# Performance work log

Hardware: AMD Instinct MI355X
Metric: run time of the kernel (lower is better)

Reference implementation:

```python
import jax, jax.numpy as jnp
import numpy as np

E = 32          # num_experts
K = 4           # num_experts_per_tok
H = 1024        # hidden_size
I = 768         # moe_intermediate_size
ROUTED_SCALING_FACTOR = 1.0


def setup_inputs() -> dict:
    key = jax.random.key(0)
    k0, k1, k2, k3, k4, k5 = jax.random.split(key, 6)
    return {
        "hidden_states": jax.random.normal(k0, (1, 2048, H), jnp.float32),
        "gate_w": jax.random.normal(k1, (E, H), jnp.float32) * 0.02,
        "w1": jax.random.normal(k2, (E, H, I), jnp.float32) * 0.02,   # gate proj per expert
        "w3": jax.random.normal(k3, (E, H, I), jnp.float32) * 0.02,   # up proj per expert
        "w2": jax.random.normal(k4, (E, I, H), jnp.float32) * 0.02,   # down proj per expert
        "e_bias": jax.random.normal(k5, (E,), jnp.float32) * 0.02,    # e_score_correction_bias
    }


def reference(hidden_states, gate_w, w1, w3, w2, e_bias):
    orig_shape = hidden_states.shape
    x = hidden_states.reshape(-1, orig_shape[-1])            # [T, H]
    T = x.shape[0]

    # ----- router gate (ReplicatedLinear, no bias) -----
    router_logits = x @ gate_w.T                             # [T, E]

    # ----- grouped top-k with num_expert_group=1, topk_group=1 == plain top-k
    # scoring_func='sigmoid'; correction bias only affects expert *selection*,
    # the routing weights are the uncorrected sigmoid scores.
    scores = jax.nn.sigmoid(router_logits.astype(jnp.float32))          # [T, E]
    _, topk_ids = jax.lax.top_k(scores + e_bias[None, :], K)            # [T, K]
    topk_w = jnp.take_along_axis(scores, topk_ids, axis=1)              # [T, K]
    # renormalize (norm_topk_prob=True)
    topk_w = topk_w / jnp.sum(topk_w, axis=1, keepdims=True)

    # dense combine weights [T, E] (zero for unselected experts)
    combine = jnp.zeros((T, E), jnp.float32).at[jnp.arange(T)[:, None], topk_ids].add(topk_w)

    # ----- experts: SwiGLU per expert, combine weighted -----
    g = jnp.einsum("th,ehi->tei", x, w1)                     # [T, E, I]
    u = jnp.einsum("th,ehi->tei", x, w3)                     # [T, E, I]
    a = jax.nn.silu(g) * u * combine[:, :, None].astype(x.dtype)
    out = jnp.einsum("tei,eih->th", a, w2)                   # [T, H]

    out = out * ROUTED_SCALING_FACTOR
    return out.reshape(orig_shape)
```

## Files before the change

### kernel.cpp

```cpp
#include <hip/hip_runtime.h>
#include <cstdint>

#define TOK 2048
#define HD  1024
#define ID  768
#define NE  32

typedef unsigned short u16t;
typedef unsigned int   u32t;
typedef __bf16 bf16x8 __attribute__((ext_vector_type(8)));
typedef float  f32x4  __attribute__((ext_vector_type(4)));
typedef u16t   u16x8  __attribute__((ext_vector_type(8)));
typedef u16t   u16x4  __attribute__((ext_vector_type(4)));
typedef float  fvec4  __attribute__((ext_vector_type(4)));

__device__ __forceinline__ u16t f2b(float f) {
  u32t u = __float_as_uint(f);
  u32t r = u + 0x7fffu + ((u >> 16) & 1u);
  return (u16t)(r >> 16);
}

__device__ __forceinline__ int swz(int row, int kc) {
  return (row * 4 + (kc ^ ((row >> 2) & 3))) * 8;
}

__global__ void k_cvt(const float* __restrict__ x, u16t* __restrict__ xb) {
  int i = (blockIdx.x * 256 + threadIdx.x) * 4;
  fvec4 v = *(const fvec4*)(x + i);
  u16x4 o = { f2b(v[0]), f2b(v[1]), f2b(v[2]), f2b(v[3]) };
  *(u16x4*)(xb + i) = o;
}

__global__ void k_router(const float* __restrict__ x, const float* __restrict__ gw,
                         const float* __restrict__ eb,
                         int* __restrict__ topk_ids, float* __restrict__ topk_w,
                         int* __restrict__ counts) {
  int lane = threadIdx.x & 63;
  int t = blockIdx.x * 4 + (threadIdx.x >> 6);
  const float* xt = x + (size_t)t * HD;
  float myscore = 0.f;
  for (int e = 0; e < NE; ++e) {
    const float* ge = gw + (size_t)e * HD;
    float s = 0.f;
#pragma unroll
    for (int i = 0; i < HD / 64; ++i) s = fmaf(xt[lane + i * 64], ge[lane + i * 64], s);
#pragma unroll
    for (int off = 32; off; off >>= 1) s += __shfl_xor(s, off);
    if (lane == e) myscore = s;
  }
  float sig = 1.f / (1.f + expf(-myscore));
  float biased = (lane < NE) ? (sig + eb[lane]) : -3.0e38f;
  float wsum = 0.f;
  int ids[4]; float wsv[4];
#pragma unroll
  for (int k = 0; k < 4; ++k) {
    float v = biased; int idx = lane;
#pragma unroll
    for (int off = 32; off; off >>= 1) {
      float ov = __shfl_xor(v, off);
      int   oi = __shfl_xor(idx, off);
      if (ov > v || (ov == v && oi < idx)) { v = ov; idx = oi; }
    }
    ids[k] = idx;
    float sc = __shfl(sig, idx);
    wsv[k] = sc; wsum += sc;
    if (lane == idx) biased = -3.0e38f;
  }
  float inv = 1.f / wsum;
#pragma unroll
  for (int k = 0; k < 4; ++k) {
    if (lane == k) {
      topk_ids[t * 4 + k] = ids[k];
      topk_w[t * 4 + k]  = wsv[k] * inv;
      atomicAdd(&counts[ids[k]], 1);
    }
  }
}

__global__ void k_bucket(const int* __restrict__ topk_ids, const float* __restrict__ topk_w,
                         const int* __restrict__ counts, int* __restrict__ offsets,
                         int* __restrict__ pairTok, float* __restrict__ pairW,
                         int* __restrict__ invp) {
  __shared__ int soff[NE + 1];
  __shared__ int scur[NE];
  int tid = threadIdx.x;
  if (tid == 0) {
    int acc = 0;
    for (int e = 0; e < NE; ++e) { soff[e] = acc; acc += counts[e]; }
    soff[NE] = acc;
  }
  if (tid < NE) scur[tid] = 0;
  __syncthreads();
  if (tid <= NE) offsets[tid] = soff[tid];
  for (int p = tid; p < TOK * 4; p += 256) {
    int e = topk_ids[p];
    int pos = soff[e] + atomicAdd(&scur[e], 1);
    pairTok[pos] = p;
    pairW[pos]   = topk_w[p];
    invp[p]      = pos;
  }
}

__launch_bounds__(256, 2)
__global__ void k_gemm1(const u16t* __restrict__ xb, const float* __restrict__ w1,
                        const float* __restrict__ w3,
                        const int* __restrict__ counts, const int* __restrict__ offsets,
                        const int* __restrict__ pairTok, const float* __restrict__ pairW,
                        u16t* __restrict__ A) {
  const int e = blockIdx.y;
  const int colbase = blockIdx.x * 64;
  const int count = counts[e];
  const int base  = offsets[e];
  const int tid = threadIdx.x, lane = tid & 63, wv = tid >> 6;

  __shared__ __align__(16) u16t Xs[256 * 32];
  __shared__ __align__(16) u16t Ws2[2][64 * 32];
  __shared__ float pw[256];
  __shared__ int   prow[256];

  const float* w1e = w1 + (size_t)e * HD * ID;
  const float* w3e = w3 + (size_t)e * HD * ID;

  for (int r0 = 0; r0 < count; r0 += 256) {
    __syncthreads();
    {
      int idx = r0 + tid;
      bool valid = idx < count;
      prow[tid] = valid ? (pairTok[base + idx] >> 2) : -1;
      pw[tid]   = valid ? pairW[base + idx] : 0.f;
    }
    f32x4 zz = {0.f, 0.f, 0.f, 0.f};
    f32x4 accg[4][4], accu[4][4];
#pragma unroll
    for (int a = 0; a < 4; ++a)
#pragma unroll
      for (int b = 0; b < 4; ++b) { accg[a][b] = zz; accu[a][b] = zz; }

    for (int kk = 0; kk < HD; kk += 32) {
      {
        int tok = prow[tid];
        u16x8 d0 = {0,0,0,0,0,0,0,0}, d1 = d0, d2 = d0, d3 = d0;
        if (tok >= 0) {
          const u16t* src = xb + (size_t)tok * HD + kk;
          d0 = *(const u16x8*)(src);
          d1 = *(const u16x8*)(src + 8);
          d2 = *(const u16x8*)(src + 16);
          d3 = *(const u16x8*)(src + 24);
        }
        *(u16x8*)&Xs[swz(tid, 0)] = d0;
        *(u16x8*)&Xs[swz(tid, 1)] = d1;
        *(u16x8*)&Xs[swz(tid, 2)] = d2;
        *(u16x8*)&Xs[swz(tid, 3)] = d3;
      }
      {
        const float* wp = (tid < 128) ? w1e : w3e;
        u16t* wsp = &Ws2[tid >> 7][0];
        int u = tid & 127;
        int cg = u & 15, hg = u >> 4;
        const float* src = wp + (size_t)(kk + hg * 4) * ID + colbase + cg * 4;
        fvec4 v0 = *(const fvec4*)(src);
        fvec4 v1 = *(const fvec4*)(src + ID);
        fvec4 v2 = *(const fvec4*)(src + 2 * ID);
        fvec4 v3 = *(const fvec4*)(src + 3 * ID);
        int kc = hg >> 1, half = (hg & 1) * 4;
#pragma unroll
        for (int c = 0; c < 4; ++c) {
          int col = cg * 4 + c;
          u16x4 pk = { f2b(v0[c]), f2b(v1[c]), f2b(v2[c]), f2b(v3[c]) };
          *(u16x4*)&wsp[swz(col, kc) + half] = pk;
        }
      }
      __syncthreads();
      bf16x8 af[4], b1f[4], b3f[4];
      int kcl = lane >> 4;
      int rb = wv * 64 + (lane & 15);
#pragma unroll
      for (int rf = 0; rf < 4; ++rf)
        af[rf] = *(const bf16x8*)&Xs[swz(rb + rf * 16, kcl)];
#pragma unroll
      for (int cf = 0; cf < 4; ++cf) {
        int col = cf * 16 + (lane & 15);
        b1f[cf] = *(const bf16x8*)&Ws2[0][swz(col, kcl)];
        b3f[cf] = *(const bf16x8*)&Ws2[1][swz(col, kcl)];
      }
#pragma unroll
      for (int rf = 0; rf < 4; ++rf)
#pragma unroll
        for (int cf = 0; cf < 4; ++cf) {
          accg[rf][cf] = __builtin_amdgcn_mfma_f32_16x16x32_bf16(af[rf], b1f[cf], accg[rf][cf], 0, 0, 0);
          accu[rf][cf] = __builtin_amdgcn_mfma_f32_16x16x32_bf16(af[rf], b3f[cf], accu[rf][cf], 0, 0, 0);
        }
      __syncthreads();
    }
#pragma unroll
    for (int rf = 0; rf < 4; ++rf) {
#pragma unroll
      for (int ri = 0; ri < 4; ++ri) {
        int rowl = wv * 64 + rf * 16 + (lane >> 4) * 4 + ri;
        int grow = r0 + rowl;
        if (grow < count) {
          float wgt = pw[rowl];
#pragma unroll
          for (int cf = 0; cf < 4; ++cf) {
            float gg = accg[rf][cf][ri];
            float uu = accu[rf][cf][ri];
            float a = gg / (1.f + expf(-gg)) * uu * wgt;
            A[(size_t)(base + grow) * ID + colbase + cf * 16 + (lane & 15)] = f2b(a);
          }
        }
      }
    }
  }
}

__launch_bounds__(256, 2)
__global__ void k_gemm2(const u16t* __restrict__ A, const float* __restrict__ w2,
                        const int* __restrict__ counts, const int* __restrict__ offsets,
                        float* __restrict__ buf) {
  const int e = blockIdx.y;
  const int colbase = blockIdx.x * 64;
  const int count = counts[e];
  const int base  = offsets[e];
  const int tid = threadIdx.x, lane = tid & 63, wv = tid >> 6;

  __shared__ __align__(16) u16t As[256 * 32];
  __shared__ __align__(16) u16t W2s[64 * 32];

  const float* w2e = w2 + (size_t)e * ID * HD;

  for (int r0 = 0; r0 < count; r0 += 256) {
    f32x4 zz = {0.f, 0.f, 0.f, 0.f};
    f32x4 acc[4][4];
#pragma unroll
    for (int a = 0; a < 4; ++a)
#pragma unroll
      for (int b = 0; b < 4; ++b) acc[a][b] = zz;

    for (int kk = 0; kk < ID; kk += 32) {
      {
        int idx = r0 + tid;
        u16x8 d0 = {0,0,0,0,0,0,0,0}, d1 = d0, d2 = d0, d3 = d0;
        if (idx < count) {
          const u16t* src = A + (size_t)(base + idx) * ID + kk;
          d0 = *(const u16x8*)(src);
          d1 = *(const u16x8*)(src + 8);
          d2 = *(const u16x8*)(src + 16);
          d3 = *(const u16x8*)(src + 24);
        }
        *(u16x8*)&As[swz(tid, 0)] = d0;
        *(u16x8*)&As[swz(tid, 1)] = d1;
        *(u16x8*)&As[swz(tid, 2)] = d2;
        *(u16x8*)&As[swz(tid, 3)] = d3;
      }
      {
        int cg = tid & 15, kg = tid >> 4;
        const float* src = w2e + (size_t)(kk + kg * 2) * HD + colbase + cg * 4;
        fvec4 v0 = *(const fvec4*)(src);
        fvec4 v1 = *(const fvec4*)(src + HD);
        int k0 = kg * 2;
        int kc = k0 >> 3, off = k0 & 7;
#pragma unroll
        for (int c = 0; c < 4; ++c) {
          int col = cg * 4 + c;
          u32t pk = (u32t)f2b(v0[c]) | ((u32t)f2b(v1[c]) << 16);
          *(u32t*)&W2s[swz(col, kc) + off] = pk;
        }
      }
      __syncthreads();
      bf16x8 af[4], bf[4];
      int kcl = lane >> 4;
      int rb = wv * 64 + (lane & 15);
#pragma unroll
      for (int rf = 0; rf < 4; ++rf)
        af[rf] = *(const bf16x8*)&As[swz(rb + rf * 16, kcl)];
#pragma unroll
      for (int cf = 0; cf < 4; ++cf)
        bf[cf] = *(const bf16x8*)&W2s[swz(cf * 16 + (lane & 15), kcl)];
#pragma unroll
      for (int rf = 0; rf < 4; ++rf)
#pragma unroll
        for (int cf = 0; cf < 4; ++cf)
          acc[rf][cf] = __builtin_amdgcn_mfma_f32_16x16x32_bf16(af[rf], bf[cf], acc[rf][cf], 0, 0, 0);
      __syncthreads();
    }
#pragma unroll
    for (int rf = 0; rf < 4; ++rf)
#pragma unroll
      for (int ri = 0; ri < 4; ++ri) {
        int rowl = wv * 64 + rf * 16 + (lane >> 4) * 4 + ri;
        int grow = r0 + rowl;
        if (grow < count) {
#pragma unroll
          for (int cf = 0; cf < 4; ++cf)
            buf[(size_t)(base + grow) * HD + colbase + cf * 16 + (lane & 15)] = acc[rf][cf][ri];
        }
      }
  }
}

__global__ void k_reduce(const float* __restrict__ buf, const int* __restrict__ invp,
                         float* __restrict__ out) {
  int t = blockIdx.x;
  int col = threadIdx.x * 4;
  int p0 = invp[t * 4 + 0], p1 = invp[t * 4 + 1];
  int p2 = invp[t * 4 + 2], p3 = invp[t * 4 + 3];
  fvec4 s = *(const fvec4*)(buf + (size_t)p0 * HD + col);
  s += *(const fvec4*)(buf + (size_t)p1 * HD + col);
  s += *(const fvec4*)(buf + (size_t)p2 * HD + col);
  s += *(const fvec4*)(buf + (size_t)p3 * HD + col);
  *(fvec4*)(out + (size_t)t * HD + col) = s;
}

extern "C" void kernel_launch(void* const* d_in, const int* in_sizes, int n_in,
                              void* d_out, int out_size, void* d_ws, size_t ws_size,
                              hipStream_t stream) {
  const float* x  = (const float*)d_in[0];
  const float* gw = (const float*)d_in[1];
  const float* w1 = (const float*)d_in[2];
  const float* w3 = (const float*)d_in[3];
  const float* w2 = (const float*)d_in[4];
  const float* eb = (const float*)d_in[5];
  float* out = (float*)d_out;

  char* ws = (char*)d_ws;
  int*   counts   = (int*)(ws);
  int*   offsets  = (int*)(ws + 256);
  int*   topk_ids = (int*)(ws + 4096);
  float* topk_w   = (float*)(ws + 36864);
  int*   pairTok  = (int*)(ws + 69632);
  float* pairW    = (float*)(ws + 102400);
  int*   invp     = (int*)(ws + 135168);
  u16t*  xb       = (u16t*)(ws + 262144);
  u16t*  Abuf     = (u16t*)(ws + 262144 + 4194304);
  float* buf      = (float*)(ws + 262144 + 4194304 + 12582912);

  hipMemsetAsync(counts, 0, 4096, stream);
  k_cvt   <<<2048, 256, 0, stream>>>(x, xb);
  k_router<<<512, 256, 0, stream>>>(x, gw, eb, topk_ids, topk_w, counts);
  k_bucket<<<1, 256, 0, stream>>>(topk_ids, topk_w, counts, offsets, pairTok, pairW, invp);
  k_gemm1 <<<dim3(12, 32), 256, 0, stream>>>(xb, w1, w3, counts, offsets, pairTok, pairW, Abuf);
  k_gemm2 <<<dim3(16, 32), 256, 0, stream>>>(Abuf, w2, counts, offsets, buf);
  k_reduce<<<2048, 256, 0, stream>>>(buf, invp, out);
}
```

Baseline: 274.7 us.

## Prefetch next K-tile into registers and split expert rows across grid z

Both expert GEMMs now issue the global loads for the next K-slice into registers before computing on the current one. This overlaps memory latency with MFMA work at the cost of extra registers. The row loop is also spread over a third grid dimension of four, so each expert's 256-row tiles run in separate blocks and more of the GPU stays busy, though each extra block re-reads the expert weights. The router is rewritten to hold x in registers and read the gate weights with vectorized float4 loads.

```diff
diff --git a/kernel.cpp b/kernel.cpp
--- a/kernel.cpp
+++ b/kernel.cpp
@@ -5,6 +5,7 @@
 #define HD  1024
 #define ID  768
 #define NE  32
+#define RT  4
 
 typedef unsigned short u16t;
 typedef unsigned int   u32t;
@@ -38,12 +39,19 @@
   int lane = threadIdx.x & 63;
   int t = blockIdx.x * 4 + (threadIdx.x >> 6);
   const float* xt = x + (size_t)t * HD;
+  fvec4 xr[4];
+#pragma unroll
+  for (int i = 0; i < 4; ++i) xr[i] = *(const fvec4*)(xt + lane * 4 + i * 256);
   float myscore = 0.f;
   for (int e = 0; e < NE; ++e) {
-    const float* ge = gw + (size_t)e * HD;
+    const float* ge = gw + (size_t)e * HD + lane * 4;
     float s = 0.f;
 #pragma unroll
-    for (int i = 0; i < HD / 64; ++i) s = fmaf(xt[lane + i * 64], ge[lane + i * 64], s);
+    for (int i = 0; i < 4; ++i) {
+      fvec4 g = *(const fvec4*)(ge + i * 256);
+      s = fmaf(xr[i][0], g[0], s); s = fmaf(xr[i][1], g[1], s);
+      s = fmaf(xr[i][2], g[2], s); s = fmaf(xr[i][3], g[3], s);
+    }
 #pragma unroll
     for (int off = 32; off; off >>= 1) s += __shfl_xor(s, off);
     if (lane == e) myscore = s;
@@ -116,19 +124,37 @@
   __shared__ __align__(16) u16t Xs[256 * 32];
   __shared__ __align__(16) u16t Ws2[2][64 * 32];
   __shared__ float pw[256];
-  __shared__ int   prow[256];
-
-  const float* w1e = w1 + (size_t)e * HD * ID;
-  const float* w3e = w3 + (size_t)e * HD * ID;
-
-  for (int r0 = 0; r0 < count; r0 += 256) {
+
+  const float* wp = (tid < 128) ? (w1 + (size_t)e * HD * ID)
+                                : (w3 + (size_t)e * HD * ID);
+  u16t* wsp = &Ws2[tid >> 7][0];
+  const int u  = tid & 127;
+  const int cg = u & 15, hg = u >> 4;
+  const int kc = hg >> 1, half = (hg & 1) * 4;
+
+  for (int r0 = blockIdx.z * 256; r0 < count; r0 += RT * 256) {
     __syncthreads();
+    int idx = r0 + tid;
+    bool valid = idx < count;
+    int pr = valid ? (pairTok[base + idx] >> 2) : -1;
+    pw[tid] = valid ? pairW[base + idx] : 0.f;
+
+    u16x8 xd[4];
+    fvec4 wd[4];
     {
-      int idx = r0 + tid;
-      bool valid = idx < count;
-      prow[tid] = valid ? (pairTok[base + idx] >> 2) : -1;
-      pw[tid]   = valid ? pairW[base + idx] : 0.f;
-    }
+      if (pr >= 0) {
+        const u16t* s = xb + (size_t)pr * HD;
+        xd[0] = *(const u16x8*)(s);      xd[1] = *(const u16x8*)(s + 8);
+        xd[2] = *(const u16x8*)(s + 16); xd[3] = *(const u16x8*)(s + 24);
+      } else {
+        u16x8 z = {0,0,0,0,0,0,0,0};
+        xd[0] = z; xd[1] = z; xd[2] = z; xd[3] = z;
+      }
+      const float* s = wp + (size_t)(hg * 4) * ID + colbase + cg * 4;
+      wd[0] = *(const fvec4*)(s);          wd[1] = *(const fvec4*)(s + ID);
+      wd[2] = *(const fvec4*)(s + 2 * ID); wd[3] = *(const fvec4*)(s + 3 * ID);
+    }
+
     f32x4 zz = {0.f, 0.f, 0.f, 0.f};
     f32x4 accg[4][4], accu[4][4];
 #pragma unroll
@@ -137,61 +163,46 @@
       for (int b = 0; b < 4; ++b) { accg[a][b] = zz; accu[a][b] = zz; }
 
     for (int kk = 0; kk < HD; kk += 32) {
-      {
-        int tok = prow[tid];
-        u16x8 d0 = {0,0,0,0,0,0,0,0}, d1 = d0, d2 = d0, d3 = d0;
-        if (tok >= 0) {
-          const u16t* src = xb + (size_t)tok * HD + kk;
-          d0 = *(const u16x8*)(src);
-          d1 = *(const u16x8*)(src + 8);
-          d2 = *(const u16x8*)(src + 16);
-          d3 = *(const u16x8*)(src + 24);
-        }
-        *(u16x8*)&Xs[swz(tid, 0)] = d0;
-        *(u16x8*)&Xs[swz(tid, 1)] = d1;
-        *(u16x8*)&Xs[swz(tid, 2)] = d2;
-        *(u16x8*)&Xs[swz(tid, 3)] = d3;
-      }
-      {
-        const float* wp = (tid < 128) ? w1e : w3e;
-        u16t* wsp = &Ws2[tid >> 7][0];
-        int u = tid & 127;
-        int cg = u & 15, hg = u >> 4;
-        const float* src = wp + (size_t)(kk + hg * 4) * ID + colbase + cg * 4;
-        fvec4 v0 = *(const fvec4*)(src);
-        fvec4 v1 = *(const fvec4*)(src + ID);
-        fvec4 v2 = *(const fvec4*)(src + 2 * ID);
-        fvec4 v3 = *(const fvec4*)(src + 3 * ID);
-        int kc = hg >> 1, half = (hg & 1) * 4;
-#pragma unroll
-        for (int c = 0; c < 4; ++c) {
-          int col = cg * 4 + c;
-          u16x4 pk = { f2b(v0[c]), f2b(v1[c]), f2b(v2[c]), f2b(v3[c]) };
-          *(u16x4*)&wsp[swz(col, kc) + half] = pk;
-        }
-      }
       __syncthreads();
-      bf16x8 af[4], b1f[4], b3f[4];
-      int kcl = lane >> 4;
-      int rb = wv * 64 + (lane & 15);
+      *(u16x8*)&Xs[swz(tid, 0)] = xd[0];
+      *(u16x8*)&Xs[swz(tid, 1)] = xd[1];
+      *(u16x8*)&Xs[swz(tid, 2)] = xd[2];
+      *(u16x8*)&Xs[swz(tid, 3)] = xd[3];
+#pragma unroll
+      for (int c = 0; c < 4; ++c) {
+        u16x4 pk = { f2b(wd[0][c]), f2b(wd[1][c]), f2b(wd[2][c]), f2b(wd[3][c]) };
+        *(u16x4*)&wsp[swz(cg * 4 + c, kc) + half] = pk;
+      }
+      __syncthreads();
+      if (kk + 32 < HD) {
+        if (pr >= 0) {
+          const u16t* s = xb + (size_t)pr * HD + kk + 32;
+          xd[0] = *(const u16x8*)(s);      xd[1] = *(const u16x8*)(s + 8);
+          xd[2] = *(const u16x8*)(s + 16); xd[3] = *(const u16x8*)(s + 24);
+        }
+        const float* s = wp + (size_t)(kk + 32 + hg * 4) * ID + colbase + cg * 4;
+        wd[0] = *(const fvec4*)(s);          wd[1] = *(const fvec4*)(s + ID);
+        wd[2] = *(const fvec4*)(s + 2 * ID); wd[3] = *(const fvec4*)(s + 3 * ID);
+      }
+      const int kcl = lane >> 4;
+      const int rb = wv * 64 + (lane & 15);
+      bf16x8 af[4];
 #pragma unroll
       for (int rf = 0; rf < 4; ++rf)
         af[rf] = *(const bf16x8*)&Xs[swz(rb + rf * 16, kcl)];
 #pragma unroll
       for (int cf = 0; cf < 4; ++cf) {
         int col = cf * 16 + (lane & 15);
-        b1f[cf] = *(const bf16x8*)&Ws2[0][swz(col, kcl)];
-        b3f[cf] = *(const bf16x8*)&Ws2[1][swz(col, kcl)];
-      }
-#pragma unroll
-      for (int rf = 0; rf < 4; ++rf)
-#pragma unroll
-        for (int cf = 0; cf < 4; ++cf) {
-          accg[rf][cf] = __builtin_amdgcn_mfma_f32_16x16x32_bf16(af[rf], b1f[cf], accg[rf][cf], 0, 0, 0);
-          accu[rf][cf] = __builtin_amdgcn_mfma_f32_16x16x32_bf16(af[rf], b3f[cf], accu[rf][cf], 0, 0, 0);
-        }
-      __syncthreads();
-    }
+        bf16x8 b1f = *(const bf16x8*)&Ws2[0][swz(col, kcl)];
+        bf16x8 b3f = *(const bf16x8*)&Ws2[1][swz(col, kcl)];
+#pragma unroll
+        for (int rf = 0; rf < 4; ++rf) {
+          accg[rf][cf] = __builtin_amdgcn_mfma_f32_16x16x32_bf16(af[rf], b1f, accg[rf][cf], 0, 0, 0);
+          accu[rf][cf] = __builtin_amdgcn_mfma_f32_16x16x32_bf16(af[rf], b3f, accu[rf][cf], 0, 0, 0);
+        }
+      }
+    }
+    __syncthreads();
 #pragma unroll
     for (int rf = 0; rf < 4; ++rf) {
 #pragma unroll
@@ -227,8 +238,28 @@
   __shared__ __align__(16) u16t W2s[64 * 32];
 
   const float* w2e = w2 + (size_t)e * ID * HD;
-
-  for (int r0 = 0; r0 < count; r0 += 256) {
+  const int cg = tid & 15, kg = tid >> 4;
+  const int k0 = kg * 2, kcw = k0 >> 3, offw = k0 & 7;
+
+  for (int r0 = blockIdx.z * 256; r0 < count; r0 += RT * 256) {
+    int idx = r0 + tid;
+    bool valid = idx < count;
+    const u16t* asrc = A + (size_t)(base + idx) * ID;
+
+    u16x8 xd[4];
+    fvec4 wd0, wd1;
+    {
+      if (valid) {
+        xd[0] = *(const u16x8*)(asrc);      xd[1] = *(const u16x8*)(asrc + 8);
+        xd[2] = *(const u16x8*)(asrc + 16); xd[3] = *(const u16x8*)(asrc + 24);
+      } else {
+        u16x8 z = {0,0,0,0,0,0,0,0};
+        xd[0] = z; xd[1] = z; xd[2] = z; xd[3] = z;
+      }
+      const float* s = w2e + (size_t)(kg * 2) * HD + colbase + cg * 4;
+      wd0 = *(const fvec4*)(s); wd1 = *(const fvec4*)(s + HD);
+    }
+
     f32x4 zz = {0.f, 0.f, 0.f, 0.f};
     f32x4 acc[4][4];
 #pragma unroll
@@ -237,51 +268,39 @@
       for (int b = 0; b < 4; ++b) acc[a][b] = zz;
 
     for (int kk = 0; kk < ID; kk += 32) {
-      {
-        int idx = r0 + tid;
-        u16x8 d0 = {0,0,0,0,0,0,0,0}, d1 = d0, d2 = d0, d3 = d0;
-        if (idx < count) {
-          const u16t* src = A + (size_t)(base + idx) * ID + kk;
-          d0 = *(const u16x8*)(src);
-          d1 = *(const u16x8*)(src + 8);
-          d2 = *(const u16x8*)(src + 16);
-          d3 = *(const u16x8*)(src + 24);
-        }
-        *(u16x8*)&As[swz(tid, 0)] = d0;
-        *(u16x8*)&As[swz(tid, 1)] = d1;
-        *(u16x8*)&As[swz(tid, 2)] = d2;
-        *(u16x8*)&As[swz(tid, 3)] = d3;
-      }
-      {
-        int cg = tid & 15, kg = tid >> 4;
-        const float* src = w2e + (size_t)(kk + kg * 2) * HD + colbase + cg * 4;
-        fvec4 v0 = *(const fvec4*)(src);
-        fvec4 v1 = *(const fvec4*)(src + HD);
-        int k0 = kg * 2;
-        int kc = k0 >> 3, off = k0 & 7;
-#pragma unroll
-        for (int c = 0; c < 4; ++c) {
-          int col = cg * 4 + c;
-          u32t pk = (u32t)f2b(v0[c]) | ((u32t)f2b(v1[c]) << 16);
-          *(u32t*)&W2s[swz(col, kc) + off] = pk;
-        }
-      }
       __syncthreads();
-      bf16x8 af[4], bf[4];
-      int kcl = lane >> 4;
-      int rb = wv * 64 + (lane & 15);
+      *(u16x8*)&As[swz(tid, 0)] = xd[0];
+      *(u16x8*)&As[swz(tid, 1)] = xd[1];
+      *(u16x8*)&As[swz(tid, 2)] = xd[2];
+      *(u16x8*)&As[swz(tid, 3)] = xd[3];
+#pragma unroll
+      for (int c = 0; c < 4; ++c) {
+        u32t pk = (u32t)f2b(wd0[c]) | ((u32t)f2b(wd1[c]) << 16);
+        *(u32t*)&W2s[swz(cg * 4 + c, kcw) + offw] = pk;
+      }
+      __syncthreads();
+      if (kk + 32 < ID) {
+        if (valid) {
+          const u16t* s = asrc + kk + 32;
+          xd[0] = *(const u16x8*)(s);      xd[1] = *(const u16x8*)(s + 8);
+          xd[2] = *(const u16x8*)(s + 16); xd[3] = *(const u16x8*)(s + 24);
+        }
+        const float* s = w2e + (size_t)(kk + 32 + kg * 2) * HD + colbase + cg * 4;
+        wd0 = *(const fvec4*)(s); wd1 = *(const fvec4*)(s + HD);
+      }
+      const int kcl = lane >> 4;
+      const int rb = wv * 64 + (lane & 15);
+      bf16x8 af[4];
 #pragma unroll
       for (int rf = 0; rf < 4; ++rf)
         af[rf] = *(const bf16x8*)&As[swz(rb + rf * 16, kcl)];
 #pragma unroll
-      for (int cf = 0; cf < 4; ++cf)
-        bf[cf] = *(const bf16x8*)&W2s[swz(cf * 16 + (lane & 15), kcl)];
-#pragma unroll
-      for (int rf = 0; rf < 4; ++rf)
-#pragma unroll
-        for (int cf = 0; cf < 4; ++cf)
-          acc[rf][cf] = __builtin_amdgcn_mfma_f32_16x16x32_bf16(af[rf], bf[cf], acc[rf][cf], 0, 0, 0);
-      __syncthreads();
+      for (int cf = 0; cf < 4; ++cf) {
+        bf16x8 bfr = *(const bf16x8*)&W2s[swz(cf * 16 + (lane & 15), kcl)];
+#pragma unroll
+        for (int rf = 0; rf < 4; ++rf)
+          acc[rf][cf] = __builtin_amdgcn_mfma_f32_16x16x32_bf16(af[rf], bfr, acc[rf][cf], 0, 0, 0);
+      }
     }
 #pragma unroll
     for (int rf = 0; rf < 4; ++rf)
@@ -338,7 +357,7 @@
   k_cvt   <<<2048, 256, 0, stream>>>(x, xb);
   k_router<<<512, 256, 0, stream>>>(x, gw, eb, topk_ids, topk_w, counts);
   k_bucket<<<1, 256, 0, stream>>>(topk_ids, topk_w, counts, offsets, pairTok, pairW, invp);
-  k_gemm1 <<<dim3(12, 32), 256, 0, stream>>>(xb, w1, w3, counts, offsets, pairTok, pairW, Abuf);
-  k_gemm2 <<<dim3(16, 32), 256, 0, stream>>>(Abuf, w2, counts, offsets, buf);
+  k_gemm1 <<<dim3(12, 32, RT), 256, 0, stream>>>(xb, w1, w3, counts, offsets, pairTok, pairW, Abuf);
+  k_gemm2 <<<dim3(16, 32, RT), 256, 0, stream>>>(Abuf, w2, counts, offsets, buf);
   k_reduce<<<2048, 256, 0, stream>>>(buf, invp, out);
 }
```

New measurement: 241.5 us. -12.1%, faster.
